# Kernel tuning notes

Measured on AMD Instinct MI355X. Metric: run time of the kernel, lower is better.

The kernel has to match this reference:

```python
import jax, jax.numpy as jnp
import numpy as np

N, F, E = 100000, 128, 1600000


def setup_inputs() -> dict:
    key = jax.random.key(0)
    ks = jax.random.split(key, 10)
    s = 1.0 / np.sqrt(F)
    return {
        "x": jax.random.normal(ks[0], (N, F), jnp.float32),
        "edge_index": jax.random.randint(ks[1], (2, E), 0, N),
        "edge_weight": jax.random.uniform(ks[2], (E,), jnp.float32),
        # EvolveGCNO initial weight (1, F, F) -> squeezed to (F, F)
        "initial_weight": jax.random.normal(ks[3], (F, F), jnp.float32) * s,
        # torch.nn.GRU(F, F) params, gate order (r, z, n)
        "gru_w_ih": jax.random.uniform(ks[4], (3 * F, F), jnp.float32, -s, s),
        "gru_w_hh": jax.random.uniform(ks[5], (3 * F, F), jnp.float32, -s, s),
        "gru_b_ih": jax.random.uniform(ks[6], (3 * F,), jnp.float32, -s, s),
        "gru_b_hh": jax.random.uniform(ks[7], (3 * F,), jnp.float32, -s, s),
        # Linear(F, 1)
        "lin_w": jax.random.uniform(ks[8], (1, F), jnp.float32, -s, s),
        "lin_b": jax.random.uniform(ks[9], (1,), jnp.float32, -s, s),
    }


def _evolve_weight(W0, w_ih, w_hh, b_ih, b_hh):
    # One GRU step: input = W0 rows (batch=F), hidden = W0 rows (first call of EvolveGCNO)
    gi = W0 @ w_ih.T + b_ih  # (F, 3F)
    gh = W0 @ w_hh.T + b_hh
    i_r, i_z, i_n = jnp.split(gi, 3, axis=-1)
    h_r, h_z, h_n = jnp.split(gh, 3, axis=-1)
    r = jax.nn.sigmoid(i_r + h_r)
    z = jax.nn.sigmoid(i_z + h_z)
    n = jnp.tanh(i_n + r * h_n)
    return (1.0 - z) * n + z * W0  # (F, F)


def reference(x, edge_index, edge_weight, initial_weight, gru_w_ih, gru_w_hh,
              gru_b_ih, gru_b_hh, lin_w, lin_b):
    W = _evolve_weight(initial_weight, gru_w_ih, gru_w_hh, gru_b_ih, gru_b_hh)
    n_nodes = x.shape[0]
    row, col = edge_index[0], edge_index[1]  # source, target
    # gcn_norm: add self loops (weight 1), sym-normalize D^-1/2 (A+I) D^-1/2
    loop = jnp.arange(n_nodes)
    row = jnp.concatenate([row, loop])
    col = jnp.concatenate([col, loop])
    w = jnp.concatenate([edge_weight, jnp.ones((n_nodes,), x.dtype)])
    deg = jax.ops.segment_sum(w, col, num_segments=n_nodes)
    dinv = jnp.where(deg > 0, jax.lax.rsqrt(deg), 0.0)
    norm = dinv[row] * w * dinv[col]  # (E+N,)
    xw = x @ W  # (N, F)
    # gather at sources, weighted scatter-add at targets
    h = jax.ops.segment_sum(norm[:, None] * xw[row], col, num_segments=n_nodes)
    h = jax.nn.relu(h)
    return (h @ lin_w.T + lin_b)[:, 0]  # (N,)
```

## Files before the change

kernel.cpp:

```cpp
#include <hip/hip_runtime.h>

#define F 128
#define DEG_SCALE 16777216.0f
#define DEG_INV   (1.0f / 16777216.0f)
#define BUCK_BITS 7
#define BUCK_COLS 128
#define CAP 2304
#define EPT 8
#define WB_STRIDE 136

typedef _Float16 half8 __attribute__((ext_vector_type(8)));
typedef float f32x4 __attribute__((ext_vector_type(4)));

__global__ __launch_bounds__(256) void init_kernel(
    int* __restrict__ cursor, int NZ, int NBUK,
    const float* __restrict__ W0, const float* __restrict__ wih,
    const float* __restrict__ whh, const float* __restrict__ bih,
    const float* __restrict__ bhh, float* __restrict__ W) {
  __shared__ float wrow[6 * F];
  int b = blockIdx.x;
  int tid = threadIdx.x;
  if (b < NZ) {
    int i = b * 256 + tid;
    if (i < NBUK) cursor[i] = 0;
    return;
  }
  int j = b - NZ;
  for (int idx = tid; idx < 6 * F; idx += 256) {
    int g = idx >> 7, k = idx & 127;
    const float* src = (g < 3) ? (wih + (size_t)(g * F + j) * F)
                               : (whh + (size_t)((g - 3) * F + j) * F);
    wrow[idx] = src[k];
  }
  __syncthreads();
  int i = tid >> 1;
  int kh = tid & 1;
  const float* w0p = W0 + (size_t)i * F + kh * 64;
  const float* wr = wrow + kh * 64;
  float ar = 0, az = 0, an = 0, br = 0, bz = 0, bn = 0;
#pragma unroll 4
  for (int k = 0; k < 64; ++k) {
    float a = w0p[k];
    ar = fmaf(a, wr[k], ar);
    az = fmaf(a, wr[F + k], az);
    an = fmaf(a, wr[2 * F + k], an);
    br = fmaf(a, wr[3 * F + k], br);
    bz = fmaf(a, wr[4 * F + k], bz);
    bn = fmaf(a, wr[5 * F + k], bn);
  }
  ar += __shfl_xor(ar, 1); az += __shfl_xor(az, 1); an += __shfl_xor(an, 1);
  br += __shfl_xor(br, 1); bz += __shfl_xor(bz, 1); bn += __shfl_xor(bn, 1);
  if (kh == 0) {
    float gr = ar + bih[j] + br + bhh[j];
    float gz = az + bih[j + F] + bz + bhh[j + F];
    float r = 1.f / (1.f + expf(-gr));
    float z = 1.f / (1.f + expf(-gz));
    float n = tanhf(an + bih[j + 2 * F] + r * (bn + bhh[j + 2 * F]));
    W[i * F + j] = (1.f - z) * n + z * W0[(size_t)i * F + j];
  }
}

__global__ __launch_bounds__(1024) void bin_kernel(
    const int* __restrict__ row, const int* __restrict__ col,
    const float* __restrict__ ew, int* __restrict__ cursor,
    uint2* __restrict__ binned, int E, int NBUK) {
  __shared__ int cnt[1024];
  __shared__ int base[1024];
  int tid = threadIdx.x;
  cnt[tid] = 0;
  __syncthreads();
  int e0 = blockIdx.x * (1024 * EPT) + tid;
  int cc[EPT];
  int lrank[EPT];
#pragma unroll
  for (int k = 0; k < EPT; ++k) {
    int e = e0 + k * 1024;
    if (e < E) {
      cc[k] = col[e];
      lrank[k] = atomicAdd(&cnt[cc[k] >> BUCK_BITS], 1);
    } else cc[k] = -1;
  }
  __syncthreads();
  if (tid < NBUK) {
    int c = cnt[tid];
    base[tid] = c ? atomicAdd(&cursor[tid], c) : 0;
  }
  __syncthreads();
#pragma unroll
  for (int k = 0; k < EPT; ++k) {
    if (cc[k] >= 0) {
      int e = e0 + k * 1024;
      int b = cc[k] >> BUCK_BITS;
      int pos = base[b] + lrank[k];
      if (pos < CAP) {
        unsigned cl = (unsigned)(cc[k] & (BUCK_COLS - 1));
        binned[(size_t)b * CAP + pos] =
            make_uint2((unsigned)row[e] | (cl << 17), __float_as_uint(ew[e]));
      }
    }
  }
}

__global__ __launch_bounds__(256) void csr_kernel(
    const uint2* __restrict__ binned, const int* __restrict__ cursor,
    int* __restrict__ offs, float* __restrict__ dinv,
    uint2* __restrict__ pairs, int N, int NBUK) {
  __shared__ unsigned long long acc[BUCK_COLS];
  __shared__ float dinvL[BUCK_COLS];
  __shared__ int wbase[BUCK_COLS];
  __shared__ int sc[BUCK_COLS];
  __shared__ int wsum[4];
  int b = blockIdx.x;
  int tid = threadIdx.x;
  if (tid < BUCK_COLS) acc[tid] = 0ull;
  int partial = 0;
  for (int i = tid; i < b; i += 256) partial += cursor[i];
#pragma unroll
  for (int m = 32; m; m >>= 1) partial += __shfl_xor(partial, m);
  if ((tid & 63) == 0) wsum[tid >> 6] = partial;
  __syncthreads();
  int bstart = b * BUCK_COLS + wsum[0] + wsum[1] + wsum[2] + wsum[3];

  int cnt = cursor[b];
  if (cnt > CAP) cnt = CAP;
  const uint2* src = binned + (size_t)b * CAP;
  for (int i = tid; i < cnt; i += 256) {
    uint2 rec = src[i];
    int cl = rec.x >> 17;
    unsigned fx = (unsigned)(__uint_as_float(rec.y) * DEG_SCALE);
    atomicAdd(&acc[cl], ((unsigned long long)1 << 32) | (unsigned long long)fx);
  }
  __syncthreads();
  int node0 = b * BUCK_COLS;
  int cvt1 = 0;
  if (tid < BUCK_COLS) {
    unsigned long long pk = acc[tid];
    int node = node0 + tid;
    if (node < N) {
      cvt1 = (int)(pk >> 32) + 1;
      float deg = (float)(unsigned)(pk & 0xffffffffull) * DEG_INV;
      float dv = rsqrtf(deg + 1.0f);
      dinvL[tid] = dv;
      dinv[node] = dv;
    }
    sc[tid] = cvt1;
  }
  __syncthreads();
  for (int off = 1; off < BUCK_COLS; off <<= 1) {
    int x = 0;
    if (tid < BUCK_COLS && tid >= off) x = sc[tid - off];
    __syncthreads();
    if (tid < BUCK_COLS) sc[tid] += x;
    __syncthreads();
  }
  if (tid < BUCK_COLS) {
    int node = node0 + tid;
    if (node < N) {
      int abs0 = bstart + sc[tid] - cvt1;
      offs[node] = abs0;
      pairs[abs0] = make_uint2((unsigned)node << 8, __float_as_uint(dinvL[tid]));
      wbase[tid] = abs0 + 1;
    }
  }
  __syncthreads();
  for (int i = tid; i < cnt; i += 256) {
    uint2 rec = src[i];
    int cl = rec.x >> 17;
    unsigned r = rec.x & 0x1ffffu;
    float wp = __uint_as_float(rec.y) * dinvL[cl];
    int pos = atomicAdd(&wbase[cl], 1);
    pairs[pos] = make_uint2(r << 8, __float_as_uint(wp));
  }
}

__global__ __launch_bounds__(256) void norm_fix(
    uint2* __restrict__ pairs, const float* __restrict__ dinv,
    int* __restrict__ offs, int N, int total) {
  int i = blockIdx.x * 256 + threadIdx.x;
  if (i < total) {
    uint2 pr = pairs[i];
    float v = __uint_as_float(pr.y) * dinv[pr.x >> 8];
    pairs[i] = make_uint2(pr.x, __float_as_uint(v));
  } else if (i < total + 16) {
    pairs[i] = make_uint2(0u, 0u);
  }
  if (i == 0) offs[N] = total;
}

__global__ __launch_bounds__(256) void gemm_xw(
    const float* __restrict__ x, const float* __restrict__ W,
    _Float16* __restrict__ xwh, int N) {
  __shared__ _Float16 Wb[F * WB_STRIDE];
  int t = threadIdx.x;
  for (int idx = t; idx < F * F; idx += 256) {
    int k = idx >> 7, n = idx & 127;
    Wb[n * WB_STRIDE + k] = (_Float16)W[idx];
  }
  __syncthreads();

  int lane = t & 63, wave = t >> 6;
  int ln = lane & 15, q = lane >> 4;
  int rowb = blockIdx.x * 64 + wave * 16;
  int i = rowb + ln;
  int iclamp = (i < N) ? i : N - 1;
  const float* xp = x + (size_t)iclamp * F + q * 8;

  half8 a[4];
#pragma unroll
  for (int tt = 0; tt < 4; ++tt) {
    float4 v0 = *(const float4*)(xp + 32 * tt);
    float4 v1 = *(const float4*)(xp + 32 * tt + 4);
    half8 av;
    av[0] = (_Float16)v0.x; av[1] = (_Float16)v0.y;
    av[2] = (_Float16)v0.z; av[3] = (_Float16)v0.w;
    av[4] = (_Float16)v1.x; av[5] = (_Float16)v1.y;
    av[6] = (_Float16)v1.z; av[7] = (_Float16)v1.w;
    a[tt] = av;
  }

  f32x4 acc[8];
#pragma unroll
  for (int nt = 0; nt < 8; ++nt) acc[nt] = (f32x4){0.f, 0.f, 0.f, 0.f};

#pragma unroll
  for (int nt = 0; nt < 8; ++nt) {
#pragma unroll
    for (int tt = 0; tt < 4; ++tt) {
      half8 bfrag = *(const half8*)&Wb[(nt * 16 + ln) * WB_STRIDE + tt * 32 + q * 8];
      acc[nt] = __builtin_amdgcn_mfma_f32_16x16x32_f16(a[tt], bfrag, acc[nt], 0, 0, 0);
    }
  }

#pragma unroll
  for (int nt = 0; nt < 8; ++nt) {
#pragma unroll
    for (int r = 0; r < 4; ++r) {
      int rowi = rowb + q * 4 + r;
      if (rowi < N) xwh[(size_t)rowi * F + nt * 16 + ln] = (_Float16)acc[nt][r];
    }
  }
}

__global__ __launch_bounds__(256) void gather_out(
    const uint2* __restrict__ pairs, const int* __restrict__ offs,
    const char* __restrict__ xwb, const float* __restrict__ linw,
    const float* __restrict__ linb, float* __restrict__ out, int N) {
  int wave = threadIdx.x >> 6;
  int lane = threadIdx.x & 63;
  int node = blockIdx.x * 4 + wave;
  if (node >= N) return;
  int c = lane & 15;
  int q = lane >> 4;

  const char* xb = xwb + (c << 4);
  float acc[8];
#pragma unroll
  for (int j = 0; j < 8; ++j) acc[j] = 0.f;

  int start = offs[node], end = offs[node + 1];
  for (int it = start + q; it < end; it += 16) {
    uint2 p0 = pairs[it];
    uint2 p1 = pairs[it + 4];
    uint2 p2 = pairs[it + 8];
    uint2 p3 = pairs[it + 12];
    float n0 = __uint_as_float(p0.y);
    float n1 = (it + 4 < end) ? __uint_as_float(p1.y) : 0.f;
    float n2 = (it + 8 < end) ? __uint_as_float(p2.y) : 0.f;
    float n3 = (it + 12 < end) ? __uint_as_float(p3.y) : 0.f;
    half8 x0 = *(const half8*)(xb + p0.x);
    half8 x1 = *(const half8*)(xb + p1.x);
    half8 x2 = *(const half8*)(xb + p2.x);
    half8 x3 = *(const half8*)(xb + p3.x);
#pragma unroll
    for (int j = 0; j < 8; ++j) acc[j] = fmaf(n0, (float)x0[j], acc[j]);
#pragma unroll
    for (int j = 0; j < 8; ++j) acc[j] = fmaf(n1, (float)x1[j], acc[j]);
#pragma unroll
    for (int j = 0; j < 8; ++j) acc[j] = fmaf(n2, (float)x2[j], acc[j]);
#pragma unroll
    for (int j = 0; j < 8; ++j) acc[j] = fmaf(n3, (float)x3[j], acc[j]);
  }

#pragma unroll
  for (int j = 0; j < 8; ++j) {
    acc[j] += __shfl_xor(acc[j], 16);
    acc[j] += __shfl_xor(acc[j], 32);
  }

  const float4* lw4 = (const float4*)linw;
  float4 la = lw4[c * 2];
  float4 lb = lw4[c * 2 + 1];
  float p = fmaxf(acc[0], 0.f) * la.x + fmaxf(acc[1], 0.f) * la.y +
            fmaxf(acc[2], 0.f) * la.z + fmaxf(acc[3], 0.f) * la.w +
            fmaxf(acc[4], 0.f) * lb.x + fmaxf(acc[5], 0.f) * lb.y +
            fmaxf(acc[6], 0.f) * lb.z + fmaxf(acc[7], 0.f) * lb.w;
#pragma unroll
  for (int m = 8; m; m >>= 1) p += __shfl_xor(p, m);

  if (lane == 0) out[node] = p + linb[0];
}

extern "C" void kernel_launch(void* const* d_in, const int* in_sizes, int n_in,
                              void* d_out, int out_size, void* d_ws, size_t ws_size,
                              hipStream_t stream) {
  const float* x    = (const float*)d_in[0];
  const int*   ei   = (const int*)d_in[1];
  const float* ew   = (const float*)d_in[2];
  const float* W0   = (const float*)d_in[3];
  const float* wih  = (const float*)d_in[4];
  const float* whh  = (const float*)d_in[5];
  const float* bih  = (const float*)d_in[6];
  const float* bhh  = (const float*)d_in[7];
  const float* linw = (const float*)d_in[8];
  const float* linb = (const float*)d_in[9];

  int N = in_sizes[0] / F;
  int E = in_sizes[2];
  const int* row = ei;
  const int* col = ei + E;
  int NBUK = (N + BUCK_COLS - 1) / BUCK_COLS;
  int total = E + N;

  char* p = (char*)d_ws;
  auto alloc = [&](size_t bytes) {
    char* q = p;
    p += (bytes + 255) & ~(size_t)255;
    return q;
  };
  float*    W      = (float*)alloc((size_t)F * F * 4);
  int*      cursor = (int*)alloc((size_t)NBUK * 4);
  float*    dinv   = (float*)alloc((size_t)N * 4);
  int*      offs   = (int*)alloc(((size_t)N + 1) * 4);
  uint2*    binned = (uint2*)alloc((size_t)NBUK * CAP * 8);
  uint2*    pairs  = (uint2*)alloc(((size_t)total + 16) * 8);
  _Float16* xwh    = (_Float16*)alloc((size_t)N * F * 2);

  int NZ = (NBUK + 255) / 256;
  init_kernel<<<NZ + 128, 256, 0, stream>>>(cursor, NZ, NBUK, W0, wih, whh, bih,
                                            bhh, W);

  int EPB = 1024 * EPT;
  bin_kernel<<<(E + EPB - 1) / EPB, 1024, 0, stream>>>(row, col, ew, cursor, binned,
                                                       E, NBUK);
  csr_kernel<<<NBUK, 256, 0, stream>>>(binned, cursor, offs, dinv, pairs, N, NBUK);
  norm_fix<<<(total + 16 + 255) / 256, 256, 0, stream>>>(pairs, dinv, offs, N, total);

  gemm_xw<<<(N + 63) / 64, 256, 0, stream>>>(x, W, xwh, N);
  gather_out<<<(N + 3) / 4, 256, 0, stream>>>(pairs, offs, (const char*)xwh,
                                              linw, linb, (float*)d_out, N);
}
```

Measured before the change: 234.8 us.

## Split CSR build into degree and pair passes, fold source normalization in

The CSR kernel is split into a degree/offset pass and a pair-writing pass. The pair pass can then multiply in the source node's dinv directly, so the separate norm_fix pass that re-read and re-wrote all E+N pairs is removed. The padding and offs[N] writes move into init_kernel. The evolved weight is also stored transposed in fp16, so gemm_xw loads it without conversion. The cost is an extra pass over the binned records, plus a random dinv[r] gather per edge.

New measurement: 228.7 us, median of 2. 2.6% less time.

```diff
diff --git a/kernel.cpp b/kernel.cpp
--- a/kernel.cpp
+++ b/kernel.cpp
@@ -16,13 +16,18 @@
     int* __restrict__ cursor, int NZ, int NBUK,
     const float* __restrict__ W0, const float* __restrict__ wih,
     const float* __restrict__ whh, const float* __restrict__ bih,
-    const float* __restrict__ bhh, float* __restrict__ W) {
+    const float* __restrict__ bhh, _Float16* __restrict__ WTh,
+    int* __restrict__ offs, uint2* __restrict__ pairs, int N, int total) {
   __shared__ float wrow[6 * F];
   int b = blockIdx.x;
   int tid = threadIdx.x;
   if (b < NZ) {
     int i = b * 256 + tid;
     if (i < NBUK) cursor[i] = 0;
+    if (b == 0) {
+      if (tid < 16) pairs[total + tid] = make_uint2(0u, 0u);
+      if (tid == 0) offs[N] = total;
+    }
     return;
   }
   int j = b - NZ;
@@ -56,7 +61,8 @@
     float r = 1.f / (1.f + expf(-gr));
     float z = 1.f / (1.f + expf(-gz));
     float n = tanhf(an + bih[j + 2 * F] + r * (bn + bhh[j + 2 * F]));
-    W[i * F + j] = (1.f - z) * n + z * W0[(size_t)i * F + j];
+    float v = (1.f - z) * n + z * W0[(size_t)i * F + j];
+    WTh[(size_t)j * F + i] = (_Float16)v;
   }
 }
 
@@ -101,13 +107,10 @@
   }
 }
 
-__global__ __launch_bounds__(256) void csr_kernel(
+__global__ __launch_bounds__(256) void csr_deg(
     const uint2* __restrict__ binned, const int* __restrict__ cursor,
-    int* __restrict__ offs, float* __restrict__ dinv,
-    uint2* __restrict__ pairs, int N, int NBUK) {
+    int* __restrict__ offs, float* __restrict__ dinv, int N, int NBUK) {
   __shared__ unsigned long long acc[BUCK_COLS];
-  __shared__ float dinvL[BUCK_COLS];
-  __shared__ int wbase[BUCK_COLS];
   __shared__ int sc[BUCK_COLS];
   __shared__ int wsum[4];
   int b = blockIdx.x;
@@ -140,61 +143,65 @@
       cvt1 = (int)(pk >> 32) + 1;
       float deg = (float)(unsigned)(pk & 0xffffffffull) * DEG_INV;
       float dv = rsqrtf(deg + 1.0f);
-      dinvL[tid] = dv;
       dinv[node] = dv;
     }
     sc[tid] = cvt1;
   }
   __syncthreads();
   for (int off = 1; off < BUCK_COLS; off <<= 1) {
-    int x = 0;
-    if (tid < BUCK_COLS && tid >= off) x = sc[tid - off];
+    int xv = 0;
+    if (tid < BUCK_COLS && tid >= off) xv = sc[tid - off];
     __syncthreads();
-    if (tid < BUCK_COLS) sc[tid] += x;
+    if (tid < BUCK_COLS) sc[tid] += xv;
     __syncthreads();
   }
+  if (tid < BUCK_COLS) {
+    int node = node0 + tid;
+    if (node < N) offs[node] = bstart + sc[tid] - cvt1;
+  }
+}
+
+__global__ __launch_bounds__(256) void csr_pairs(
+    const uint2* __restrict__ binned, const int* __restrict__ cursor,
+    const int* __restrict__ offs, const float* __restrict__ dinv,
+    uint2* __restrict__ pairs, int N, int NBUK) {
+  __shared__ float dinvL[BUCK_COLS];
+  __shared__ int wbase[BUCK_COLS];
+  int b = blockIdx.x;
+  int tid = threadIdx.x;
+  int node0 = b * BUCK_COLS;
   if (tid < BUCK_COLS) {
     int node = node0 + tid;
     if (node < N) {
-      int abs0 = bstart + sc[tid] - cvt1;
-      offs[node] = abs0;
-      pairs[abs0] = make_uint2((unsigned)node << 8, __float_as_uint(dinvL[tid]));
-      wbase[tid] = abs0 + 1;
-    }
-  }
-  __syncthreads();
+      int o = offs[node];
+      float dv = dinv[node];
+      dinvL[tid] = dv;
+      wbase[tid] = o + 1;
+      pairs[o] = make_uint2((unsigned)node << 8, __float_as_uint(dv * dv));
+    }
+  }
+  __syncthreads();
+  int cnt = cursor[b];
+  if (cnt > CAP) cnt = CAP;
+  const uint2* src = binned + (size_t)b * CAP;
   for (int i = tid; i < cnt; i += 256) {
     uint2 rec = src[i];
     int cl = rec.x >> 17;
     unsigned r = rec.x & 0x1ffffu;
-    float wp = __uint_as_float(rec.y) * dinvL[cl];
+    float wp = (__uint_as_float(rec.y) * dinvL[cl]) * dinv[r];
     int pos = atomicAdd(&wbase[cl], 1);
     pairs[pos] = make_uint2(r << 8, __float_as_uint(wp));
   }
 }
 
-__global__ __launch_bounds__(256) void norm_fix(
-    uint2* __restrict__ pairs, const float* __restrict__ dinv,
-    int* __restrict__ offs, int N, int total) {
-  int i = blockIdx.x * 256 + threadIdx.x;
-  if (i < total) {
-    uint2 pr = pairs[i];
-    float v = __uint_as_float(pr.y) * dinv[pr.x >> 8];
-    pairs[i] = make_uint2(pr.x, __float_as_uint(v));
-  } else if (i < total + 16) {
-    pairs[i] = make_uint2(0u, 0u);
-  }
-  if (i == 0) offs[N] = total;
-}
-
 __global__ __launch_bounds__(256) void gemm_xw(
-    const float* __restrict__ x, const float* __restrict__ W,
+    const float* __restrict__ x, const _Float16* __restrict__ WT,
     _Float16* __restrict__ xwh, int N) {
   __shared__ _Float16 Wb[F * WB_STRIDE];
   int t = threadIdx.x;
   for (int idx = t; idx < F * F; idx += 256) {
-    int k = idx >> 7, n = idx & 127;
-    Wb[n * WB_STRIDE + k] = (_Float16)W[idx];
+    int n = idx >> 7, k = idx & 127;
+    Wb[n * WB_STRIDE + k] = WT[idx];
   }
   __syncthreads();
 
@@ -327,7 +334,7 @@
     p += (bytes + 255) & ~(size_t)255;
     return q;
   };
-  float*    W      = (float*)alloc((size_t)F * F * 4);
+  _Float16* WTh    = (_Float16*)alloc((size_t)F * F * 2);
   int*      cursor = (int*)alloc((size_t)NBUK * 4);
   float*    dinv   = (float*)alloc((size_t)N * 4);
   int*      offs   = (int*)alloc(((size_t)N + 1) * 4);
@@ -337,15 +344,15 @@
 
   int NZ = (NBUK + 255) / 256;
   init_kernel<<<NZ + 128, 256, 0, stream>>>(cursor, NZ, NBUK, W0, wih, whh, bih,
-                                            bhh, W);
+                                            bhh, WTh, offs, pairs, N, total);
 
   int EPB = 1024 * EPT;
   bin_kernel<<<(E + EPB - 1) / EPB, 1024, 0, stream>>>(row, col, ew, cursor, binned,
                                                        E, NBUK);
-  csr_kernel<<<NBUK, 256, 0, stream>>>(binned, cursor, offs, dinv, pairs, N, NBUK);
-  norm_fix<<<(total + 16 + 255) / 256, 256, 0, stream>>>(pairs, dinv, offs, N, total);
-
-  gemm_xw<<<(N + 63) / 64, 256, 0, stream>>>(x, W, xwh, N);
+  csr_deg<<<NBUK, 256, 0, stream>>>(binned, cursor, offs, dinv, N, NBUK);
+  csr_pairs<<<NBUK, 256, 0, stream>>>(binned, cursor, offs, dinv, pairs, N, NBUK);
+
+  gemm_xw<<<(N + 63) / 64, 256, 0, stream>>>(x, WTh, xwh, N);
   gather_out<<<(N + 3) / 4, 256, 0, stream>>>(pairs, offs, (const char*)xwh,
                                               linw, linb, (float*)d_out, N);
 }
```
